# Kernel optimization log

Measured on AMD Instinct MI355X. Metric: run time of the kernel, lower is better.

## Reference

```python
import jax, jax.numpy as jnp
import numpy as np

H = 16  # n_heads
D = 1024  # embed_dim == input_dim
FF = 4 * D
EPS = 1e-5  # torch LayerNorm default


def layer_norm(x, g, b):
    m = x.mean(-1, keepdims=True)
    v = x.var(-1, keepdims=True)
    return (x - m) / jnp.sqrt(v + EPS) * g + b


def setup_inputs() -> dict:
    key = jax.random.key(0)
    ks = jax.random.split(key, 8)
    s = lambda k, sh: (jax.random.normal(k, sh, jnp.float32) * 0.02)
    return {
        "kq": jax.random.normal(ks[0], (4, 2048, 512), jnp.float32),
        "v": jax.random.normal(ks[1], (4, 2048, 512), jnp.float32),
        "Wk": s(ks[2], (D, D)), "bk": jnp.zeros((D,), jnp.float32),
        "Wq": s(ks[3], (D, D)), "bq": jnp.zeros((D,), jnp.float32),
        "Wv": s(ks[4], (D, D)), "bv": jnp.zeros((D,), jnp.float32),
        "W1": s(ks[5], (FF, D)), "b1": jnp.zeros((FF,), jnp.float32),
        "W2": s(ks[6], (D, FF)), "b2": jnp.zeros((D,), jnp.float32),
        "g1": jnp.ones((D,), jnp.float32), "be1": jnp.zeros((D,), jnp.float32),
        "g2": jnp.ones((D,), jnp.float32), "be2": jnp.zeros((D,), jnp.float32),
    }


def reference(kq, v, Wk, bk, Wq, bq, Wv, bv, W1, b1, W2, b2, g1, be1, g2, be2):
    X = jnp.concatenate([kq, v], axis=-1)  # [n, T, input_dim]
    n, T, _ = kq.shape

    def heads(y):  # [n, T, D] -> [n, H, T, hd]
        return y.reshape(n, T, H, -1).transpose(0, 2, 1, 3)

    K = heads(X @ Wk.T + bk)
    Q = heads(X @ Wq.T + bq)
    V = heads(X @ Wv.T + bv)

    # NOTE: source applies no 1/sqrt(head_dim) scaling
    scores = jnp.einsum('nhqd,nhkd->nhqk', Q, K)
    causal = jnp.tril(jnp.ones((T, T), bool))  # mask = -inf strictly above diagonal
    scores = jnp.where(causal, scores, -jnp.inf)
    A = jax.nn.softmax(scores, axis=-1)
    attn_out = jnp.einsum('nhqk,nhkd->nhqd', A, V)
    attn_out = attn_out.transpose(0, 2, 1, 3).reshape(n, T, -1)  # [n, T, D]

    Vflat = V.transpose(0, 2, 1, 3).reshape(n, T, -1)  # residual is V projection, per source
    h = layer_norm(Vflat + attn_out, g1, be1)
    ff = jax.nn.gelu(h @ W1.T + b1, approximate=False) @ W2.T + b2  # torch GELU default = exact erf
    return layer_norm(h + ff, g2, be2)
```

## Files before the change

kernel.cpp:

```cpp
#include <hip/hip_runtime.h>
#include <stdint.h>

#define SEQ 2048
#define DM  1024
#define NH  16
#define HD  64
#define FFD 4096
#define TOK 8192

typedef __bf16 bf16x8 __attribute__((ext_vector_type(8)));
typedef float  f32x4  __attribute__((ext_vector_type(4)));
typedef float  f32x16 __attribute__((ext_vector_type(16)));
typedef unsigned short u16x8 __attribute__((ext_vector_type(8)));
typedef unsigned short u16x4 __attribute__((ext_vector_type(4)));
typedef unsigned int   u32x4 __attribute__((ext_vector_type(4)));

__device__ __forceinline__ unsigned short f2bf(float f) {
  unsigned u = __builtin_bit_cast(unsigned, f);
  u += 0x7fffu + ((u >> 16) & 1u);
  return (unsigned short)(u >> 16);
}
__device__ __forceinline__ float bf2f(unsigned short h) {
  return __builtin_bit_cast(float, ((unsigned)h) << 16);
}
__device__ __forceinline__ f32x4 mfma16(bf16x8 a, bf16x8 b, f32x4 c) {
  return __builtin_amdgcn_mfma_f32_16x16x32_bf16(a, b, c, 0, 0, 0);
}
__device__ __forceinline__ f32x16 mfma32(bf16x8 a, bf16x8 b, f32x16 c) {
  return __builtin_amdgcn_mfma_f32_32x32x16_bf16(a, b, c, 0, 0, 0);
}
__device__ __forceinline__ unsigned cvtpk(float lo, float hi) {
  unsigned r;
  asm("v_cvt_pk_bf16_f32 %0, %1, %2" : "=v"(r) : "v"(lo), "v"(hi));
  return r;
}
__device__ __forceinline__ void gld_lds16(void* lds, const void* g) {
  __builtin_amdgcn_global_load_lds((__attribute__((address_space(1))) void*)g,
                                   (__attribute__((address_space(3))) void*)lds,
                                   16, 0, 0);
}

__global__ __launch_bounds__(256) void concat_cast(
    const float* __restrict__ kq, const float* __restrict__ v,
    unsigned short* __restrict__ X) {
  int i = (blockIdx.x * 256 + threadIdx.x) * 4;
  int tkn = i >> 10;
  int c = i & 1023;
  const float* s = (c < 512) ? (kq + (size_t)tkn * 512 + c)
                             : (v  + (size_t)tkn * 512 + (c - 512));
  f32x4 f = *(const f32x4*)s;
  u16x4 o = { f2bf(f[0]), f2bf(f[1]), f2bf(f[2]), f2bf(f[3]) };
  *(u16x4*)&X[i] = o;
}

__global__ __launch_bounds__(256) void castW5(
    const float* __restrict__ Wk, const float* __restrict__ Wq,
    const float* __restrict__ Wv, const float* __restrict__ W1,
    const float* __restrict__ W2, unsigned short* __restrict__ dst1,
    unsigned short* __restrict__ dst2) {
  int e = (blockIdx.x * 256 + threadIdx.x) * 4;
  const float* src;
  unsigned short* dst;
  if (e < 3145728) {
    src = (e < 1048576) ? (Wk + e)
        : (e < 2097152) ? (Wq + (e - 1048576))
                        : (Wv + (e - 2097152));
    dst = dst1 + e;
  } else {
    int e2 = e - 3145728;
    src = (e2 < 4194304) ? (W1 + e2) : (W2 + (e2 - 4194304));
    dst = dst2 + e2;
  }
  f32x4 f = *(const f32x4*)src;
  u16x4 o = { f2bf(f[0]), f2bf(f[1]), f2bf(f[2]), f2bf(f[3]) };
  *(u16x4*)dst = o;
}

__global__ __launch_bounds__(256) void bias3(
    const float* __restrict__ a, const float* __restrict__ b,
    const float* __restrict__ c, float* __restrict__ o) {
  int i = blockIdx.x * 256 + threadIdx.x;
  if (i < 1024) o[i] = a[i];
  else if (i < 2048) o[i] = b[i - 1024];
  else if (i < 3072) o[i] = c[i - 2048];
}

template<int BM, int EPI>
__global__ __launch_bounds__(512, 2) void gemm256(
    const unsigned short* __restrict__ A, const unsigned short* __restrict__ B,
    const float* __restrict__ bias, void* __restrict__ Cout,
    void* __restrict__ CoutQ, void* __restrict__ CoutV, void* __restrict__ CoutVI,
    int M, int N, int K, int PR, int PC, int NPC) {
  constexpr int MF = BM / 32;
  constexpr int MG = MF / 4;
  extern __shared__ __align__(16) unsigned short lds[];
  unsigned short* Asm0 = lds;
  unsigned short* Bsm0 = lds + 2 * BM * 64;
  const int tid = threadIdx.x;
  const int w = tid >> 6, l = tid & 63, lr = l & 15, lg = l >> 4;
  const int wm = w >> 2, wn = w & 3;
  const int bid = blockIdx.x;
  const int xcd = bid & 7;
  const int i = bid >> 3;
  const int patch_r = xcd / NPC, patch_c = xcd % NPC;
  const int bm = (patch_r * PR + (i % PR)) * BM;
  const int bn = (patch_c * PC + (i / PR)) * 256;
  const int NT = K >> 6;
  const int srow = tid >> 3;
  const int sc8  = tid & 7;

  f32x4 acc[MF][4] = {};

  auto stage = [&](int kt, int bb) {
    unsigned short* da = Asm0 + bb * (BM * 64);
    unsigned short* db = Bsm0 + bb * (256 * 64);
#pragma unroll
    for (int p = 0; p < BM / 64; ++p) {
      int row = p * 64 + srow;
      gld_lds16(da + (p * 512 + w * 64) * 8,
                &A[(size_t)(bm + row) * K + kt * 64 + ((sc8 ^ (row & 7)) << 3)]);
    }
#pragma unroll
    for (int p = 0; p < 4; ++p) {
      int row = p * 64 + srow;
      gld_lds16(db + (p * 512 + w * 64) * 8,
                &B[(size_t)(bn + row) * K + kt * 64 + ((sc8 ^ (row & 7)) << 3)]);
    }
  };

  stage(0, 0);

  for (int t = 0; t < NT; ++t) {
    asm volatile("s_waitcnt vmcnt(0)" ::: "memory");
    __builtin_amdgcn_s_barrier();
    if (t + 1 < NT) stage(t + 1, (t + 1) & 1);
    const unsigned short* As = Asm0 + (t & 1) * (BM * 64);
    const unsigned short* Bs = Bsm0 + (t & 1) * (256 * 64);
    bf16x8 bv[4][2];
#pragma unroll
    for (int fn = 0; fn < 4; ++fn)
#pragma unroll
      for (int kk = 0; kk < 2; ++kk) {
        int row = wn * 64 + fn * 16 + lr;
        int c8 = (kk * 4 + lg) ^ (row & 7);
        bv[fn][kk] = *(const bf16x8*)&Bs[row * 64 + c8 * 8];
      }
#pragma unroll
    for (int mg = 0; mg < MG; ++mg) {
      bf16x8 av[4][2];
#pragma unroll
      for (int fr = 0; fr < 4; ++fr)
#pragma unroll
        for (int kk = 0; kk < 2; ++kk) {
          int row = wm * (BM / 2) + (mg * 4 + fr) * 16 + lr;
          int c8 = (kk * 4 + lg) ^ (row & 7);
          av[fr][kk] = *(const bf16x8*)&As[row * 64 + c8 * 8];
        }
      __builtin_amdgcn_s_setprio(1);
#pragma unroll
      for (int fr = 0; fr < 4; ++fr)
#pragma unroll
        for (int nf = 0; nf < 4; ++nf)
#pragma unroll
          for (int kk = 0; kk < 2; ++kk)
            acc[mg * 4 + fr][nf] = mfma16(av[fr][kk], bv[nf][kk], acc[mg * 4 + fr][nf]);
      __builtin_amdgcn_s_setprio(0);
    }
  }
#pragma unroll
  for (int mf = 0; mf < MF; ++mf) {
    int row0 = bm + wm * (BM / 2) + mf * 16 + lg * 4;
#pragma unroll
    for (int nf = 0; nf < 4; ++nf) {
      int col = bn + wn * 64 + nf * 16 + lr;
      float bcol = bias[col];
#pragma unroll
      for (int r = 0; r < 4; ++r) {
        float vv = acc[mf][nf][r] + bcol;
        int row = row0 + r;
        if (EPI == 2) vv = 0.5f * vv * (1.0f + erff(vv * 0.70710678118654752f));
        if (EPI == 0) {
          ((float*)Cout)[(size_t)row * N + col] = vv;
        } else if (EPI == 5) {
          int third = col >> 10, c = col & 1023;
          unsigned short hv = f2bf(vv);
          int bb = row >> 11, tt = row & 2047;
          if (third == 0) {
            int hh = c >> 6, dc = (c >> 4) & 3, dl = c & 15;
            ((unsigned short*)Cout)[((((size_t)(bb * 16 + hh) * 4 + dc) * 2048 + tt) << 4) + dl] = hv;
          } else if (third == 1) {
            ((unsigned short*)CoutQ)[(size_t)row * 1024 + c] = hv;
          } else {
            ((unsigned short*)CoutV)[(size_t)row * 1024 + c] = hv;
            int hh = c >> 6, d = c & 63;
            ((unsigned short*)CoutVI)[((((size_t)(bb * 16 + hh) * 128 + (tt >> 4)) * 64 + d) << 4) + (tt & 15)] = hv;
          }
        } else {
          ((unsigned short*)Cout)[(size_t)row * N + col] = f2bf(vv);
        }
      }
    }
  }
}

__global__ __launch_bounds__(128, 4) void attn_kernel(
    const unsigned short* __restrict__ Q, const unsigned short* __restrict__ KI,
    const unsigned short* __restrict__ VI, unsigned short* __restrict__ O) {
  __shared__ __align__(16) unsigned short T[32 * 72];
  __shared__ __align__(16) float O1f[32][68];
  __shared__ float M1[64], L1[64];
  const int tid = threadIdx.x;
  const int w = tid >> 6, l = tid & 63;
  const int q32 = l & 31;
  const int g = l >> 5;
  const int x = blockIdx.x;
  const int bh = (x & 7) * 8 + (x >> 3);
  const int b = bh >> 4, h = bh & 15;
  const int u = 63 - (int)blockIdx.y;
  const int nt = u + 1;
  const int nh = (nt + 1) >> 1;
  const int jbeg = w ? nh : 0;
  const int jend = w ? nt : nh;
  const size_t tok0 = (size_t)b * SEQ;
  const size_t hoff = (size_t)h * 64;
  const unsigned short* Kp = KI + (size_t)bh * 4 * SEQ * 16;
  const unsigned short* Vp = VI + (size_t)bh * 128 * 64 * 16;

  const int q0 = u * 32;
  const int qg = q0 + q32;

  bf16x8 qf[4];
#pragma unroll
  for (int ks = 0; ks < 4; ++ks)
    qf[ks] = *(const bf16x8*)&Q[(tok0 + qg) * DM + hoff + ks * 16 + g * 8];

  f32x16 ot0 = {}, ot1 = {};
  float m = -3.0e38f, lden = 0.f;

  if (jbeg < jend) {
    bf16x8 kf[4], vf[4];
#pragma unroll
    for (int ks = 0; ks < 4; ++ks)
      kf[ks] = *(const bf16x8*)&Kp[((size_t)ks * SEQ + jbeg * 32 + q32) * 16 + g * 8];
#pragma unroll
    for (int dt = 0; dt < 2; ++dt)
#pragma unroll
      for (int s = 0; s < 2; ++s)
        vf[dt * 2 + s] = *(const bf16x8*)&Vp[(((size_t)jbeg * 2 + s) * 64 + dt * 32 + q32) * 16 + g * 8];

#pragma unroll 1
    for (int j = jbeg; j < jend; ++j) {
      f32x16 st = {};
      __builtin_amdgcn_s_setprio(1);
#pragma unroll
      for (int ks = 0; ks < 4; ++ks) st = mfma32(kf[ks], qf[ks], st);
      __builtin_amdgcn_s_setprio(0);
      const int jn = (j + 1 < jend) ? j + 1 : j;
      bf16x8 kn[4], vn[4];
#pragma unroll
      for (int ks = 0; ks < 4; ++ks)
        kn[ks] = *(const bf16x8*)&Kp[((size_t)ks * SEQ + jn * 32 + q32) * 16 + g * 8];
#pragma unroll
      for (int dt = 0; dt < 2; ++dt)
#pragma unroll
        for (int s = 0; s < 2; ++s)
          vn[dt * 2 + s] = *(const bf16x8*)&Vp[(((size_t)jn * 2 + s) * 64 + dt * 32 + q32) * 16 + g * 8];
      if (j == u) {
#pragma unroll
        for (int r = 0; r < 16; ++r) {
          int kg = j * 32 + (r & 3) + 8 * (r >> 2) + 4 * g;
          if (kg > qg) st[r] = -3.0e38f;
        }
      }
      float x0 = fmaxf(st[0], st[1]),  x1 = fmaxf(st[2], st[3]);
      float x2 = fmaxf(st[4], st[5]),  x3 = fmaxf(st[6], st[7]);
      float x4 = fmaxf(st[8], st[9]),  x5 = fmaxf(st[10], st[11]);
      float x6 = fmaxf(st[12], st[13]), x7 = fmaxf(st[14], st[15]);
      x0 = fmaxf(x0, x1); x2 = fmaxf(x2, x3); x4 = fmaxf(x4, x5); x6 = fmaxf(x6, x7);
      x0 = fmaxf(x0, x2); x4 = fmaxf(x4, x6);
      float pmax = fmaxf(x0, x4);
      if (__any(pmax - m > 8.0f)) {
        float pp = fmaxf(pmax, __shfl_xor(pmax, 32, 64));
        float mnew = fmaxf(m, pp);
        float sc = __expf(m - mnew);
#pragma unroll
        for (int r = 0; r < 16; ++r) { ot0[r] *= sc; ot1[r] *= sc; }
        lden *= sc;
        m = mnew;
      }
      float p[16];
#pragma unroll
      for (int r = 0; r < 16; ++r) p[r] = __expf(st[r] - m);
      {
        float s0 = p[0] + p[1], s1 = p[2] + p[3], s2 = p[4] + p[5], s3 = p[6] + p[7];
        float s4 = p[8] + p[9], s5 = p[10] + p[11], s6 = p[12] + p[13], s7 = p[14] + p[15];
        s0 += s1; s2 += s3; s4 += s5; s6 += s7;
        s0 += s2; s4 += s6;
        lden += s0 + s4;
      }
      unsigned c0 = cvtpk(p[0], p[1]),   c1 = cvtpk(p[2], p[3]);
      unsigned c2 = cvtpk(p[4], p[5]),   c3 = cvtpk(p[6], p[7]);
      unsigned c4 = cvtpk(p[8], p[9]),   c5 = cvtpk(p[10], p[11]);
      unsigned c6 = cvtpk(p[12], p[13]), c7 = cvtpk(p[14], p[15]);
      unsigned y0 = __shfl_xor(c0, 32, 64), y1 = __shfl_xor(c1, 32, 64);
      unsigned y2 = __shfl_xor(c2, 32, 64), y3 = __shfl_xor(c3, 32, 64);
      unsigned y4 = __shfl_xor(c4, 32, 64), y5 = __shfl_xor(c5, 32, 64);
      unsigned y6 = __shfl_xor(c6, 32, 64), y7 = __shfl_xor(c7, 32, 64);
      u32x4 f0 = { g ? y2 : c0, g ? y3 : c1, g ? c2 : y0, g ? c3 : y1 };
      u32x4 f1 = { g ? y6 : c4, g ? y7 : c5, g ? c6 : y4, g ? c7 : y5 };
      bf16x8 pb0 = __builtin_bit_cast(bf16x8, f0);
      bf16x8 pb1 = __builtin_bit_cast(bf16x8, f1);
      __builtin_amdgcn_s_setprio(1);
      ot0 = mfma32(vf[0], pb0, ot0);
      ot0 = mfma32(vf[1], pb1, ot0);
      ot1 = mfma32(vf[2], pb0, ot1);
      ot1 = mfma32(vf[3], pb1, ot1);
      __builtin_amdgcn_s_setprio(0);
#pragma unroll
      for (int ks = 0; ks < 4; ++ks) kf[ks] = kn[ks];
#pragma unroll
      for (int q = 0; q < 4; ++q) vf[q] = vn[q];
    }
  }
  if (w == 1) {
#pragma unroll
    for (int r = 0; r < 16; ++r) {
      O1f[r][l]      = ot0[r];
      O1f[16 + r][l] = ot1[r];
    }
    M1[l] = m;
    L1[l] = lden;
  }
  __syncthreads();
  if (w == 0) {
    float m1 = M1[l], l1c = L1[l];
    float mN = fmaxf(m, m1);
    float s0 = __expf(m - mN), s1 = __expf(m1 - mN);
    lden = lden * s0 + l1c * s1;
    lden += __shfl_xor(lden, 32, 64);
    float inv = 1.0f / lden;
#pragma unroll
    for (int r = 0; r < 16; ++r) {
      ot0[r] = ot0[r] * s0 + O1f[r][l] * s1;
      ot1[r] = ot1[r] * s0 + O1f[16 + r][l] * s1;
    }
#pragma unroll
    for (int r = 0; r < 16; ++r) {
      int d = (r & 3) + 8 * (r >> 2) + 4 * g;
      T[q32 * 72 + d]      = f2bf(ot0[r] * inv);
      T[q32 * 72 + 32 + d] = f2bf(ot1[r] * inv);
    }
#pragma unroll
    for (int j2 = 0; j2 < 4; ++j2) {
      int col = g * 32 + j2 * 8;
      u16x8 vv = *(const u16x8*)&T[q32 * 72 + col];
      *(u16x8*)&O[(tok0 + q0 + q32) * DM + hoff + col] = vv;
    }
  }
}

template<int MODE>
__global__ __launch_bounds__(256) void ln_kernel(
    const unsigned short* __restrict__ Xa, const void* __restrict__ Xc,
    const float* __restrict__ g, const float* __restrict__ be,
    void* __restrict__ outp) {
  const int row = blockIdx.x, t = threadIdx.x;
  const size_t base = (size_t)row * DM + t * 4;
  float x[4];
  u16x4 a = *(const u16x4*)&Xa[base];
  if (MODE == 0) {
    u16x4 c = *(const u16x4*)&((const unsigned short*)Xc)[base];
#pragma unroll
    for (int i = 0; i < 4; ++i) x[i] = bf2f(a[i]) + bf2f(c[i]);
  } else {
    f32x4 c = *(const f32x4*)&((const float*)Xc)[base];
#pragma unroll
    for (int i = 0; i < 4; ++i) x[i] = bf2f(a[i]) + c[i];
  }
  float s = x[0] + x[1] + x[2] + x[3];
  float ss = x[0] * x[0] + x[1] * x[1] + x[2] * x[2] + x[3] * x[3];
#pragma unroll
  for (int m = 1; m < 64; m <<= 1) {
    s  += __shfl_xor(s, m, 64);
    ss += __shfl_xor(ss, m, 64);
  }
  __shared__ float red[8];
  const int w = t >> 6;
  if ((t & 63) == 0) { red[w * 2] = s; red[w * 2 + 1] = ss; }
  __syncthreads();
  s  = red[0] + red[2] + red[4] + red[6];
  ss = red[1] + red[3] + red[5] + red[7];
  const float mean = s * (1.0f / DM);
  const float var = ss * (1.0f / DM) - mean * mean;
  const float rstd = rsqrtf(var + 1e-5f);
  if (MODE == 0) {
    u16x4 o;
#pragma unroll
    for (int i = 0; i < 4; ++i) {
      int cx = t * 4 + i;
      o[i] = f2bf((x[i] - mean) * rstd * g[cx] + be[cx]);
    }
    *(u16x4*)&((unsigned short*)outp)[base] = o;
  } else {
    f32x4 o;
#pragma unroll
    for (int i = 0; i < 4; ++i) {
      int cx = t * 4 + i;
      o[i] = (x[i] - mean) * rstd * g[cx] + be[cx];
    }
    *(f32x4*)&((float*)outp)[base] = o;
  }
}

extern "C" void kernel_launch(void* const* d_in, const int* in_sizes, int n_in,
                              void* d_out, int out_size, void* d_ws, size_t ws_size,
                              hipStream_t stream) {
  (void)in_sizes; (void)n_in; (void)out_size; (void)ws_size;
  const float* kq  = (const float*)d_in[0];
  const float* v   = (const float*)d_in[1];
  const float* Wk  = (const float*)d_in[2];
  const float* bk  = (const float*)d_in[3];
  const float* Wq  = (const float*)d_in[4];
  const float* bq  = (const float*)d_in[5];
  const float* Wv  = (const float*)d_in[6];
  const float* bv  = (const float*)d_in[7];
  const float* W1  = (const float*)d_in[8];
  const float* b1  = (const float*)d_in[9];
  const float* W2  = (const float*)d_in[10];
  const float* b2  = (const float*)d_in[11];
  const float* g1  = (const float*)d_in[12];
  const float* be1 = (const float*)d_in[13];
  const float* g2  = (const float*)d_in[14];
  const float* be2 = (const float*)d_in[15];
  float* out = (float*)d_out;
  uint8_t* ws = (uint8_t*)d_ws;

  unsigned short* Xb   = (unsigned short*)(ws + 0);
  unsigned short* Wkb  = (unsigned short*)(ws + 16777216);
  unsigned short* Qb   = (unsigned short*)(ws + 23068672);
  unsigned short* Kb   = (unsigned short*)(ws + 39845888);
  unsigned short* Ab   = (unsigned short*)(ws + 56623104);
  unsigned short* F1b  = (unsigned short*)(ws + 0);
  unsigned short* W1b  = (unsigned short*)(ws + 73400320);
  unsigned short* Vb   = (unsigned short*)(ws + 90177536);
  unsigned short* Hb   = (unsigned short*)(ws + 106954752);
  float*          F2f  = (float*)(ws + 123731968);
  unsigned short* VIg  = (unsigned short*)(ws + 123731968);
  float*          bqkv = (float*)(ws + 140509184);
  unsigned short* W2b  = W1b + 4194304;

  concat_cast<<<TOK * DM / 1024, 256, 0, stream>>>(kq, v, Xb);
  castW5<<<11264, 256, 0, stream>>>(Wk, Wq, Wv, W1, W2, Wkb, W1b);
  bias3<<<12, 256, 0, stream>>>(bk, bq, bv, bqkv);

  gemm256<128, 5><<<768, 512, 98304, stream>>>(
      Xb, Wkb, bqkv, Kb, Qb, Vb, VIg, TOK, 3072, DM, 8, 12, 1);

  attn_kernel<<<dim3(64, 64), 128, 0, stream>>>(Qb, Kb, VIg, Ab);

  ln_kernel<0><<<TOK, 256, 0, stream>>>(Vb, Ab, g1, be1, Hb);

  gemm256<256, 2><<<512, 512, 131072, stream>>>(
      Hb, W1b, b1, F1b, nullptr, nullptr, nullptr, TOK, FFD, DM, 8, 8, 2);
  gemm256<128, 0><<<256, 512, 98304, stream>>>(
      F1b, W2b, b2, F2f, nullptr, nullptr, nullptr, TOK, DM, FFD, 8, 4, 1);

  ln_kernel<1><<<TOK, 256, 0, stream>>>(Hb, F2f, g2, be2, out);
}
```

Baseline: 368.9 us.

## Split GEMM K-step into four quadrant phases with staggered prefetch waits

Each 64-wide K step of the bf16 GEMM is split into four quadrant sub-phases (an A half paired with a B half). The next tile's loads are issued per quadrant, and partial `s_waitcnt vmcnt` waits replace the single full drain, so compute can start once its quadrant has landed. The LDS layout is remapped so each quadrant is contiguous. This aims to overlap global-to-LDS traffic with MFMA work more finely, at the cost of extra barriers per K step and more complex indexing.

```diff
diff --git a/kernel.cpp b/kernel.cpp
--- a/kernel.cpp
+++ b/kernel.cpp
@@ -86,13 +86,13 @@
 }
 
 template<int BM, int EPI>
-__global__ __launch_bounds__(512, 2) void gemm256(
+__global__ __launch_bounds__(512, 2) void gemm4p(
     const unsigned short* __restrict__ A, const unsigned short* __restrict__ B,
     const float* __restrict__ bias, void* __restrict__ Cout,
     void* __restrict__ CoutQ, void* __restrict__ CoutV, void* __restrict__ CoutVI,
     int M, int N, int K, int PR, int PC, int NPC) {
-  constexpr int MF = BM / 32;
-  constexpr int MG = MF / 4;
+  constexpr int MF  = BM / 32;
+  constexpr int MFH = MF / 2;
   extern __shared__ __align__(16) unsigned short lds[];
   unsigned short* Asm0 = lds;
   unsigned short* Bsm0 = lds + 2 * BM * 64;
@@ -111,59 +111,86 @@
 
   f32x4 acc[MF][4] = {};
 
-  auto stage = [&](int kt, int bb) {
-    unsigned short* da = Asm0 + bb * (BM * 64);
-    unsigned short* db = Bsm0 + bb * (256 * 64);
-#pragma unroll
-    for (int p = 0; p < BM / 64; ++p) {
-      int row = p * 64 + srow;
-      gld_lds16(da + (p * 512 + w * 64) * 8,
-                &A[(size_t)(bm + row) * K + kt * 64 + ((sc8 ^ (row & 7)) << 3)]);
-    }
-#pragma unroll
-    for (int p = 0; p < 4; ++p) {
-      int row = p * 64 + srow;
-      gld_lds16(db + (p * 512 + w * 64) * 8,
-                &B[(size_t)(bn + row) * K + kt * 64 + ((sc8 ^ (row & 7)) << 3)]);
+  auto stageU = [&](int kt, int bb, int u) {
+    const int sub = u >> 1;
+    if (u & 1) {
+      unsigned short* da = Asm0 + bb * (BM * 64);
+      if constexpr (BM == 256) {
+#pragma unroll
+        for (int p = 0; p < 2; ++p) {
+          int ldr = sub * 128 + p * 64 + srow;
+          int grow = ((ldr >> 6) & 1) * 128 + sub * 64 + (ldr & 63);
+          gld_lds16(da + (sub * 128 + p * 64) * 64 + tid * 8,
+                    &A[(size_t)(bm + grow) * K + kt * 64 + ((sc8 ^ (srow & 7)) << 3)]);
+        }
+      } else {
+        int ldr = sub * 64 + srow;
+        int grow = ((ldr >> 5) & 1) * 64 + sub * 32 + (ldr & 31);
+        gld_lds16(da + sub * 4096 + tid * 8,
+                  &A[(size_t)(bm + grow) * K + kt * 64 + ((sc8 ^ (srow & 7)) << 3)]);
+      }
+    } else {
+      unsigned short* db = Bsm0 + bb * (256 * 64);
+#pragma unroll
+      for (int p = 0; p < 2; ++p) {
+        int ldr = sub * 128 + p * 64 + srow;
+        int grow = ((ldr >> 5) & 3) * 64 + sub * 32 + (ldr & 31);
+        gld_lds16(db + (sub * 128 + p * 64) * 64 + tid * 8,
+                  &B[(size_t)(bn + grow) * K + kt * 64 + ((sc8 ^ (srow & 7)) << 3)]);
+      }
     }
   };
 
-  stage(0, 0);
+#pragma unroll
+  for (int u = 0; u < 4; ++u) stageU(0, 0, u);
 
   for (int t = 0; t < NT; ++t) {
-    asm volatile("s_waitcnt vmcnt(0)" ::: "memory");
-    __builtin_amdgcn_s_barrier();
-    if (t + 1 < NT) stage(t + 1, (t + 1) & 1);
-    const unsigned short* As = Asm0 + (t & 1) * (BM * 64);
-    const unsigned short* Bs = Bsm0 + (t & 1) * (256 * 64);
-    bf16x8 bv[4][2];
-#pragma unroll
-    for (int fn = 0; fn < 4; ++fn)
-#pragma unroll
-      for (int kk = 0; kk < 2; ++kk) {
-        int row = wn * 64 + fn * 16 + lr;
-        int c8 = (kk * 4 + lg) ^ (row & 7);
-        bv[fn][kk] = *(const bf16x8*)&Bs[row * 64 + c8 * 8];
-      }
-#pragma unroll
-    for (int mg = 0; mg < MG; ++mg) {
-      bf16x8 av[4][2];
-#pragma unroll
-      for (int fr = 0; fr < 4; ++fr)
+    const int cur = t & 1;
+    const bool pre = (t + 1 < NT);
+    const unsigned short* As = Asm0 + cur * (BM * 64);
+    const unsigned short* Bs = Bsm0 + cur * (256 * 64);
+#pragma unroll
+    for (int q = 0; q < 4; ++q) {
+      if (q == 0) {
+        if (pre) {
+          if constexpr (BM == 256) asm volatile("s_waitcnt vmcnt(4)" ::: "memory");
+          else                     asm volatile("s_waitcnt vmcnt(3)" ::: "memory");
+        } else {
+          asm volatile("s_waitcnt vmcnt(0)" ::: "memory");
+        }
+        __builtin_amdgcn_s_barrier();
+      } else if (q < 3 && pre) {
+        if constexpr (BM == 256) asm volatile("s_waitcnt vmcnt(4)" ::: "memory");
+        else                     asm volatile("s_waitcnt vmcnt(3)" ::: "memory");
+        __builtin_amdgcn_s_barrier();
+      }
+      if (pre) stageU(t + 1, cur ^ 1, q);
+      bf16x8 av[MFH][2], bv[2][2];
+#pragma unroll
+      for (int f2 = 0; f2 < 2; ++f2)
 #pragma unroll
         for (int kk = 0; kk < 2; ++kk) {
-          int row = wm * (BM / 2) + (mg * 4 + fr) * 16 + lr;
-          int c8 = (kk * 4 + lg) ^ (row & 7);
-          av[fr][kk] = *(const bf16x8*)&As[row * 64 + c8 * 8];
+          int ldr = (q & 1) * 128 + wn * 32 + f2 * 16 + lr;
+          bv[f2][kk] = *(const bf16x8*)&Bs[ldr * 64 + (((kk * 4 + lg) ^ (lr & 7)) << 3)];
+        }
+#pragma unroll
+      for (int fr = 0; fr < MFH; ++fr)
+#pragma unroll
+        for (int kk = 0; kk < 2; ++kk) {
+          int ldr = (BM == 256) ? ((q >> 1) * 128 + wm * 64 + fr * 16 + lr)
+                                : ((q >> 1) * 64 + wm * 32 + fr * 16 + lr);
+          av[fr][kk] = *(const bf16x8*)&As[ldr * 64 + (((kk * 4 + lg) ^ (lr & 7)) << 3)];
         }
       __builtin_amdgcn_s_setprio(1);
 #pragma unroll
-      for (int fr = 0; fr < 4; ++fr)
-#pragma unroll
-        for (int nf = 0; nf < 4; ++nf)
+      for (int fr = 0; fr < MFH; ++fr)
+#pragma unroll
+        for (int f2 = 0; f2 < 2; ++f2)
 #pragma unroll
           for (int kk = 0; kk < 2; ++kk)
-            acc[mg * 4 + fr][nf] = mfma16(av[fr][kk], bv[nf][kk], acc[mg * 4 + fr][nf]);
+            acc[(q >> 1) * MFH + fr][(q & 1) * 2 + f2] =
+                mfma16(av[fr][kk], bv[f2][kk],
+                       acc[(q >> 1) * MFH + fr][(q & 1) * 2 + f2]);
       __builtin_amdgcn_s_setprio(0);
     }
   }
@@ -453,16 +480,16 @@
   castW5<<<11264, 256, 0, stream>>>(Wk, Wq, Wv, W1, W2, Wkb, W1b);
   bias3<<<12, 256, 0, stream>>>(bk, bq, bv, bqkv);
 
-  gemm256<128, 5><<<768, 512, 98304, stream>>>(
+  gemm4p<128, 5><<<768, 512, 98304, stream>>>(
       Xb, Wkb, bqkv, Kb, Qb, Vb, VIg, TOK, 3072, DM, 8, 12, 1);
 
   attn_kernel<<<dim3(64, 64), 128, 0, stream>>>(Qb, Kb, VIg, Ab);
 
   ln_kernel<0><<<TOK, 256, 0, stream>>>(Vb, Ab, g1, be1, Hb);
 
-  gemm256<256, 2><<<512, 512, 131072, stream>>>(
+  gemm4p<256, 2><<<512, 512, 131072, stream>>>(
       Hb, W1b, b1, F1b, nullptr, nullptr, nullptr, TOK, FFD, DM, 8, 8, 2);
-  gemm256<128, 0><<<256, 512, 98304, stream>>>(
+  gemm4p<128, 0><<<256, 512, 98304, stream>>>(
       F1b, W2b, b2, F2f, nullptr, nullptr, nullptr, TOK, DM, FFD, 8, 4, 1);
 
   ln_kernel<1><<<TOK, 256, 0, stream>>>(Hb, F2f, g2, be2, out);
```

Result: slower. 386.0 us (+4.7%).
